# Optimization experiments

Measured on AMD Instinct MI355X. Metric: run time of the kernel, lower is better.

The kernel has to match this reference:

```python
import jax, jax.numpy as jnp
import numpy as np

B, S, H, D = 4, 2048, 12, 64
HIDDEN = H * D  # 768
WINDOW = 64     # config.local_attention // 2
ROPE_THETA = 10000.0  # local_rope_theta for sliding layers


def rotate_half(x):
    d = x.shape[-1] // 2
    return jnp.concatenate([-x[..., d:], x[..., :d]], axis=-1)


def setup_inputs() -> dict:
    key = jax.random.key(0)
    k1, k2, k3 = jax.random.split(key, 3)
    hidden_states = jax.random.normal(k1, (B, S, HIDDEN), dtype=jnp.float32)
    # RoPE tables (HF style): inv_freq over half dims, duplicated
    inv_freq = 1.0 / (ROPE_THETA ** (jnp.arange(0, D, 2, dtype=jnp.float32) / D))  # [D/2]
    pos = jnp.arange(S, dtype=jnp.float32)
    freqs = pos[:, None] * inv_freq[None, :]          # [S, D/2]
    emb = jnp.concatenate([freqs, freqs], axis=-1)    # [S, D]
    cos = jnp.broadcast_to(jnp.cos(emb)[None], (B, S, D))
    sin = jnp.broadcast_to(jnp.sin(emb)[None], (B, S, D))
    # sliding-window additive mask [B,1,S,S]
    idx = jnp.arange(S)
    allowed = jnp.abs(idx[:, None] - idx[None, :]) <= WINDOW
    neg = jnp.finfo(jnp.float32).min
    attention_mask = jnp.broadcast_to(
        jnp.where(allowed, 0.0, neg)[None, None], (B, 1, S, S)
    ).astype(jnp.float32)
    std = 0.02
    Wqkv_w = jax.random.normal(k2, (3 * HIDDEN, HIDDEN), dtype=jnp.float32) * std
    Wo_w = jax.random.normal(k3, (HIDDEN, HIDDEN), dtype=jnp.float32) * std
    return {"hidden_states": hidden_states, "cos": cos, "sin": sin,
            "attention_mask": attention_mask, "Wqkv_w": Wqkv_w, "Wo_w": Wo_w}


def reference(hidden_states, cos, sin, attention_mask, Wqkv_w, Wo_w):
    b, s, _ = hidden_states.shape
    scaling = D ** -0.5
    qkv = hidden_states @ Wqkv_w.T                       # [B,S,3*HIDDEN]
    qkv = qkv.reshape(b, s, 3, H, D)
    q = jnp.transpose(qkv[:, :, 0], (0, 2, 1, 3))        # [B,H,S,D]
    k = jnp.transpose(qkv[:, :, 1], (0, 2, 1, 3))
    v = jnp.transpose(qkv[:, :, 2], (0, 2, 1, 3))
    # RoPE with float32 intermediates (inputs already fp32 here)
    c = cos[:, None].astype(jnp.float32)                 # [B,1,S,D]
    sn = sin[:, None].astype(jnp.float32)
    qf, kf = q.astype(jnp.float32), k.astype(jnp.float32)
    q = (qf * c + rotate_half(qf) * sn).astype(q.dtype)
    k = (kf * c + rotate_half(kf) * sn).astype(k.dtype)
    # SDPA with explicit additive mask
    scores = jnp.einsum('bhqd,bhkd->bhqk', q, k) * scaling + attention_mask
    attn = jax.nn.softmax(scores, axis=-1)
    out = jnp.einsum('bhqk,bhkd->bhqd', attn, v)         # [B,H,S,D]
    out = jnp.transpose(out, (0, 2, 1, 3)).reshape(b, s, HIDDEN)
    return out @ Wo_w.T
```

## Files before the change

kernel.cpp:

```cpp
#include <hip/hip_runtime.h>
#include <math.h>


typedef __attribute__((ext_vector_type(8))) short short8;
typedef __attribute__((ext_vector_type(4))) float floatx4;

constexpr int kB = 4;
constexpr int kS = 2048;
constexpr int kH = 12;
constexpr int kD = 64;
constexpr int kHidden = 768;
constexpr int kQKV = 3 * kHidden;

__device__ __forceinline__ unsigned short f2bf(float f) {
  union { float f; unsigned int u; } x; x.f = f;
  unsigned int r = (x.u + 0x7fffu + ((x.u >> 16) & 1u)) >> 16;
  return (unsigned short)r;
}

__global__ __launch_bounds__(256) void cvt_all(
    const float* __restrict__ h, const float* __restrict__ wqkv,
    const float* __restrict__ wo, unsigned short* __restrict__ hb,
    unsigned short* __restrict__ wqb, unsigned short* __restrict__ wob) {
  constexpr int n1 = kB * kS * kHidden / 4;
  constexpr int n2 = kQKV * kHidden / 4;
  constexpr int n3 = kHidden * kHidden / 4;
  int i = blockIdx.x * 256 + threadIdx.x;
  const float* src;
  unsigned short* dst;
  if (i < n1) {
    src = h; dst = hb;
  } else if (i < n1 + n2) {
    i -= n1; src = wqkv; dst = wqb;
  } else {
    i -= n1 + n2; if (i >= n3) return; src = wo; dst = wob;
  }
  const float4 v = ((const float4*)src)[i];
  ushort4 o;
  o.x = f2bf(v.x); o.y = f2bf(v.y); o.z = f2bf(v.z); o.w = f2bf(v.w);
  ((ushort4*)dst)[i] = o;
}

__device__ __forceinline__ void gload_lds16(const unsigned short* g, unsigned short* l) {
  __builtin_amdgcn_global_load_lds(
      (const __attribute__((address_space(1))) unsigned int*)g,
      (__attribute__((address_space(3))) unsigned int*)l, 16, 0, 0);
}

__global__ __launch_bounds__(512) void gemm_qkv(
    const unsigned short* __restrict__ A,
    const unsigned short* __restrict__ B,
    const float* __restrict__ cosp, const float* __restrict__ sinp,
    unsigned short* __restrict__ Qr, unsigned short* __restrict__ Kr,
    unsigned short* __restrict__ Vt) {
  constexpr int K = kHidden;
  constexpr int NP = 2 * (K / 64);
  __shared__ unsigned short SH[128 * 136];
  unsigned short* Ah0 = SH;
  unsigned short* Ah1 = SH + 4096;
  unsigned short* Bh0 = SH + 8192;
  unsigned short* Bh1 = SH + 12288;

  const int tid = threadIdx.x;
  const int lane = tid & 63;
  const int wave = tid >> 6;
  const int m0 = blockIdx.x * 128;
  const int n0 = blockIdx.y * 128;

  const int sc = wave * 64 + lane;
  const int srow = sc >> 2;
  const int sgc = ((sc & 3) ^ ((srow >> 1) & 3)) * 8;
  const int ldsOff = sc * 8;
  const unsigned short* gA0 = A + (size_t)(m0 + srow) * K + sgc;
  const unsigned short* gB0 = B + (size_t)(n0 + srow) * K + sgc;

  const int wm = wave >> 1, wn = wave & 1;
  const int mr = wm * 32 + (lane & 15);
  const int nr = wn * 64 + (lane & 15);
  const int kq = lane >> 4;

  int aOff[2], bOff[4];
#pragma unroll
  for (int i = 0; i < 2; i++) {
    const int r = mr + i * 16;
    aOff[i] = (r * 4 + (kq ^ ((r >> 1) & 3))) * 8;
  }
#pragma unroll
  for (int j = 0; j < 4; j++) {
    const int r = nr + j * 16;
    bOff[j] = (r * 4 + (kq ^ ((r >> 1) & 3))) * 8;
  }

  floatx4 acc[2][4];
#pragma unroll
  for (int i = 0; i < 2; i++)
#pragma unroll
    for (int j = 0; j < 4; j++) acc[i][j] = (floatx4)(0.f);

  gload_lds16(gA0, &Ah0[ldsOff]);
  gload_lds16(gB0, &Bh0[ldsOff]);

  for (int p = 0; p < NP; ++p) {
    if (p + 1 < NP) {
      const int kn = ((p + 1) >> 1) * 64 + ((p + 1) & 1) * 32;
      unsigned short* Ad = ((p + 1) & 1) ? Ah1 : Ah0;
      unsigned short* Bd = ((p + 1) & 1) ? Bh1 : Bh0;
      gload_lds16(gA0 + kn, &Ad[ldsOff]);
      gload_lds16(gB0 + kn, &Bd[ldsOff]);
      asm volatile("s_waitcnt vmcnt(2)" ::: "memory");
    } else {
      asm volatile("s_waitcnt vmcnt(0)" ::: "memory");
    }
    __builtin_amdgcn_s_barrier();
    __builtin_amdgcn_sched_barrier(0);
    const unsigned short* Asb = (p & 1) ? Ah1 : Ah0;
    const unsigned short* Bsb = (p & 1) ? Bh1 : Bh0;
    short8 af[2], bf[4];
#pragma unroll
    for (int i = 0; i < 2; i++) af[i] = *(const short8*)&Asb[aOff[i]];
#pragma unroll
    for (int j = 0; j < 4; j++) bf[j] = *(const short8*)&Bsb[bOff[j]];
#pragma unroll
    for (int i = 0; i < 2; i++)
#pragma unroll
      for (int j = 0; j < 4; j++)
        acc[i][j] = __builtin_amdgcn_mfma_f32_16x16x32_bf16(af[i], bf[j],
                                                            acc[i][j], 0, 0, 0);
    __builtin_amdgcn_sched_barrier(0);
    __builtin_amdgcn_s_barrier();
  }

  unsigned short (*Obuf)[136] = (unsigned short (*)[136])SH;

  const int region = n0 / kHidden;
  const int b = m0 >> 11, s0 = m0 & 2047;
  const int h0 = (n0 % kHidden) >> 6;
  const int rowL0 = wm * 32 + kq * 4;

  if (region == 2) {
#pragma unroll
    for (int i = 0; i < 2; i++)
#pragma unroll
      for (int r = 0; r < 4; r++) {
        const int rowL = rowL0 + i * 16 + r;
#pragma unroll
        for (int j = 0; j < 4; j++)
          Obuf[wn * 64 + j * 16 + (lane & 15)][rowL] = f2bf(acc[i][j][r]);
      }
    __syncthreads();
#pragma unroll
    for (int it = 0; it < 4; it++) {
      const int t = tid + it * 512;
      const int s8 = t & 15, rowc = t >> 4;
      const int hl = rowc >> 6, d = rowc & 63;
      *(short8*)(Vt + ((size_t)(b * kH + h0 + hl) * kD + d) * kS + s0 + s8 * 8) =
          *(const short8*)&Obuf[rowc][s8 * 8];
    }
  } else {
    unsigned short* dst = (region == 0) ? Qr : Kr;
    const float qscale = (region == 0) ? 0.125f : 1.f;
#pragma unroll
    for (int i = 0; i < 2; i++)
#pragma unroll
      for (int r = 0; r < 4; r++) {
        const int rowL = rowL0 + i * 16 + r;
        const int s = s0 + rowL;
        const float* cs = cosp + ((size_t)(b * kS + s)) * kD;
        const float* sns = sinp + ((size_t)(b * kS + s)) * kD;
#pragma unroll
        for (int jp = 0; jp < 2; jp++) {
          const int colL = wn * 64 + jp * 16 + (lane & 15);
          const int d = colL & 63;
          const float c = cs[d], sn = sns[d];
          const float xlo = acc[i][jp][r], xhi = acc[i][jp + 2][r];
          Obuf[rowL][colL]      = f2bf((xlo * c - xhi * sn) * qscale);
          Obuf[rowL][colL + 32] = f2bf((xhi * c + xlo * sn) * qscale);
        }
      }
    __syncthreads();
#pragma unroll
    for (int it = 0; it < 4; it++) {
      const int t = tid + it * 512;
      const int d8 = t & 7, sl = (t >> 3) & 127, hl = t >> 10;
      *(short8*)(dst + ((size_t)(b * kH + h0 + hl) * kS + s0 + sl) * kD + d8 * 8) =
          *(const short8*)&Obuf[sl][hl * 64 + d8 * 8];
    }
  }
}

__global__ __launch_bounds__(256) void gemm_bf16_nt(
    const unsigned short* __restrict__ A, const unsigned short* __restrict__ B,
    float* __restrict__ C, int M, int N, int K) {
  __shared__ unsigned short As[128 * 64];
  __shared__ unsigned short Bs[64 * 64];

  const int tid = threadIdx.x;
  const int lane = tid & 63;
  const int wave = tid >> 6;
  const int l15 = lane & 15;
  const int m0 = blockIdx.x * 128;
  const int n0 = blockIdx.y * 64;

  int ldsA[4];
  const unsigned short* gA[4];
#pragma unroll
  for (int t = 0; t < 4; t++) {
    const int ci = (wave * 4 + t) * 64 + lane;
    const int row = ci >> 3;
    const int c = (ci & 7) ^ (row & 7);
    ldsA[t] = ci * 8;
    gA[t] = A + (size_t)(m0 + row) * K + c * 8;
  }
  int ldsB[2];
  const unsigned short* gB[2];
#pragma unroll
  for (int t = 0; t < 2; t++) {
    const int ci = (wave * 2 + t) * 64 + lane;
    const int row = ci >> 3;
    const int c = (ci & 7) ^ (row & 7);
    ldsB[t] = ci * 8;
    gB[t] = B + (size_t)(n0 + row) * K + c * 8;
  }

  const int wm = wave >> 1, wn = wave & 1;
  const int mr = wm * 64 + l15;
  const int nr = wn * 32 + l15;
  const int kq = lane >> 4;

  floatx4 acc[4][2];
#pragma unroll
  for (int i = 0; i < 4; i++)
#pragma unroll
    for (int j = 0; j < 2; j++) acc[i][j] = (floatx4)(0.f);

  for (int k0 = 0; k0 < K; k0 += 64) {
    if (k0) __syncthreads();
#pragma unroll
    for (int t = 0; t < 4; t++) gload_lds16(gA[t] + k0, &As[ldsA[t]]);
#pragma unroll
    for (int t = 0; t < 2; t++) gload_lds16(gB[t] + k0, &Bs[ldsB[t]]);
    __syncthreads();
#pragma unroll
    for (int s = 0; s < 2; s++) {
      short8 af[4], bf[2];
#pragma unroll
      for (int i = 0; i < 4; i++)
        af[i] = *(const short8*)&As[(mr + i * 16) * 64 + (((s * 4 + kq) ^ ((mr + i * 16) & 7)) * 8)];
#pragma unroll
      for (int j = 0; j < 2; j++)
        bf[j] = *(const short8*)&Bs[(nr + j * 16) * 64 + (((s * 4 + kq) ^ ((nr + j * 16) & 7)) * 8)];
#pragma unroll
      for (int i = 0; i < 4; i++)
#pragma unroll
        for (int j = 0; j < 2; j++)
          acc[i][j] = __builtin_amdgcn_mfma_f32_16x16x32_bf16(af[i], bf[j],
                                                              acc[i][j], 0, 0, 0);
    }
  }

  const int crow = m0 + wm * 64 + kq * 4;
  const int ccol = n0 + wn * 32 + l15;
#pragma unroll
  for (int i = 0; i < 4; i++)
#pragma unroll
    for (int r = 0; r < 4; r++) {
      float* cp = C + (size_t)(crow + i * 16 + r) * N + ccol;
#pragma unroll
      for (int j = 0; j < 2; j++) cp[j * 16] = acc[i][j][r];
    }
}

constexpr int AQT = 64;

__global__ __launch_bounds__(256) void attn_v4(
    const unsigned short* __restrict__ Qr, const unsigned short* __restrict__ Kr,
    const unsigned short* __restrict__ Vt, unsigned short* __restrict__ out) {
  __shared__ unsigned short Pfrag[4][6][64][8];
  __shared__ float Ssum[2][AQT];

  const int tid = threadIdx.x;
  const int lane = tid & 63;
  const int wave = tid >> 6;
  const int quad = lane >> 4;
  const int l15 = lane & 15;
  const int qbase = blockIdx.x * AQT;
  const int h = blockIdx.y, b = blockIdx.z;
  const int bh = b * kH + h;
  const int kbase = qbase - 64;
  const int tq = wave >> 1;
  const int kh = wave & 1;

  short8 a0[2], a1[2];
#pragma unroll
  for (int qs = 0; qs < 2; qs++) {
    const unsigned short* qsrc =
        Qr + ((size_t)bh * kS + qbase + tq * 32 + qs * 16 + l15) * kD + quad * 8;
    a0[qs] = *(const short8*)qsrc;
    a1[qs] = *(const short8*)(qsrc + 32);
  }

  floatx4 acc[2][6];
  const unsigned short* ksrc = Kr + (size_t)bh * kS * kD;
#pragma unroll
  for (int g = 0; g < 6; g++) {
    int row = kbase + (kh * 6 + g) * 16 + l15;
    row = min(max(row, 0), kS - 1);
    const unsigned short* kp = ksrc + (size_t)row * kD + quad * 8;
    const short8 b0 = *(const short8*)kp;
    const short8 b1 = *(const short8*)(kp + 32);
#pragma unroll
    for (int qs = 0; qs < 2; qs++) {
      floatx4 z = (floatx4)(0.f);
      z = __builtin_amdgcn_mfma_f32_16x16x32_bf16(a0[qs], b0, z, 0, 0, 0);
      z = __builtin_amdgcn_mfma_f32_16x16x32_bf16(a1[qs], b1, z, 0, 0, 0);
      acc[qs][g] = z;
    }
  }

  short8 vf[2][6];
  {
    const unsigned short* vbase = Vt + (size_t)bh * kD * kS;
#pragma unroll
    for (int nt = 0; nt < 2; nt++) {
      const unsigned short* vrow = vbase + (size_t)(kh * 32 + nt * 16 + l15) * kS;
#pragma unroll
      for (int kk = 0; kk < 6; kk++) {
        int s0 = kbase + kk * 32 + quad * 8;
        s0 = min(max(s0, 0), kS - 8);
        vf[nt][kk] = *(const short8*)(vrow + s0);
      }
    }
  }

#pragma unroll
  for (int qs = 0; qs < 2; qs++) {
    const int qgrp = tq * 2 + qs;
#pragma unroll
    for (int r = 0; r < 4; r++) {
      const int q = tq * 32 + qs * 16 + quad * 4 + r;
      float s = 0.f;
#pragma unroll
      for (int g = 0; g < 6; g++) {
        const int key = (kh * 6 + g) * 16 + l15;
        const int kg_ = kbase + key;
        const bool valid = (key >= q) && (key <= q + 128) && (kg_ >= 0) && (kg_ < kS);
        const float e = valid ? __expf(acc[qs][g][r]) : 0.f;
        s += e;
        Pfrag[qgrp][key >> 5][((key >> 3) & 3) * 16 + quad * 4 + r][key & 7] = f2bf(e);
      }
#pragma unroll
      for (int off = 1; off < 16; off <<= 1) s += __shfl_xor(s, off, 64);
      if (l15 == 0) Ssum[kh][q] = s;
    }
  }
  __syncthreads();

  floatx4 o[2][2];
#pragma unroll
  for (int qs = 0; qs < 2; qs++)
#pragma unroll
    for (int nt = 0; nt < 2; nt++) o[qs][nt] = (floatx4)(0.f);
#pragma unroll
  for (int kk = 0; kk < 6; kk++) {
#pragma unroll
    for (int qs = 0; qs < 2; qs++) {
      const short8 pa = *(const short8*)&Pfrag[tq * 2 + qs][kk][lane][0];
      o[qs][0] = __builtin_amdgcn_mfma_f32_16x16x32_bf16(pa, vf[0][kk], o[qs][0], 0, 0, 0);
      o[qs][1] = __builtin_amdgcn_mfma_f32_16x16x32_bf16(pa, vf[1][kk], o[qs][1], 0, 0, 0);
    }
  }

  __syncthreads();
  unsigned short (*Ob)[68] = (unsigned short (*)[68])Pfrag;
#pragma unroll
  for (int qs = 0; qs < 2; qs++)
#pragma unroll
    for (int r = 0; r < 4; r++) {
      const int q = tq * 32 + qs * 16 + quad * 4 + r;
      const float inv = 1.f / (Ssum[0][q] + Ssum[1][q]);
      Ob[q][kh * 32 + l15] = f2bf(o[qs][0][r] * inv);
      Ob[q][kh * 32 + 16 + l15] = f2bf(o[qs][1][r] * inv);
    }
  __syncthreads();
#pragma unroll
  for (int it = 0; it < 2; it++) {
    const int t = tid + it * 256;
    const int q = t >> 3, d8 = t & 7;
    *(short8*)(out + ((size_t)(b * kS + qbase + q)) * kHidden + h * kD + d8 * 8) =
        *(const short8*)&Ob[q][d8 * 8];
  }
}

extern "C" void kernel_launch(void* const* d_in, const int* in_sizes, int n_in,
                              void* d_out, int out_size, void* d_ws,
                              size_t ws_size, hipStream_t stream) {
  const float* hidden = (const float*)d_in[0];
  const float* cosp = (const float*)d_in[1];
  const float* sinp = (const float*)d_in[2];
  const float* wqkv = (const float*)d_in[4];
  const float* wo = (const float*)d_in[5];
  float* out = (float*)d_out;

  const int M = kB * kS;
  const size_t szH = (size_t)M * kHidden;

  unsigned short* hbf = (unsigned short*)d_ws;
  unsigned short* wqkvbf = hbf + szH;
  unsigned short* wobf = wqkvbf + (size_t)kQKV * kHidden;
  unsigned short* attnbf = wobf + (size_t)kHidden * kHidden;
  unsigned short* Qrb = attnbf + szH;
  unsigned short* Krb = Qrb + szH;
  unsigned short* Vtb = Krb + szH;

  const int ncvt = (M * kHidden + kQKV * kHidden + kHidden * kHidden) / 4;
  cvt_all<<<(ncvt + 255) / 256, 256, 0, stream>>>(hidden, wqkv, wo, hbf,
                                                  wqkvbf, wobf);

  dim3 g1(M / 128, kQKV / 128);
  gemm_qkv<<<g1, 512, 0, stream>>>(hbf, wqkvbf, cosp, sinp, Qrb, Krb, Vtb);

  dim3 ga(kS / AQT, kH, kB);
  attn_v4<<<ga, 256, 0, stream>>>(Qrb, Krb, Vtb, attnbf);

  dim3 g2(M / 128, kHidden / 64);
  gemm_bf16_nt<<<g2, 256, 0, stream>>>(attnbf, wobf, out, M, kHidden, kHidden);
}
```

Measured before the change: 206.3 us.

## Load A fragments directly to registers and triple-buffer B in LDS

The QKV GEMM no longer stages the A (hidden states) tile through LDS. Each wave reads its A fragments straight from global memory into registers. The B tile moves to a three-slot LDS ring buffer, which lets the kernel drop the trailing barrier in every k-iteration. The aim is to cut LDS traffic and barrier count, at the cost of uncached, latency-exposed global loads for A that are duplicated across the two waves sharing rows.

```diff
diff --git a/kernel.cpp b/kernel.cpp
--- a/kernel.cpp
+++ b/kernel.cpp
@@ -56,14 +56,11 @@
   constexpr int K = kHidden;
   constexpr int NP = 2 * (K / 64);
   __shared__ unsigned short SH[128 * 136];
-  unsigned short* Ah0 = SH;
-  unsigned short* Ah1 = SH + 4096;
-  unsigned short* Bh0 = SH + 8192;
-  unsigned short* Bh1 = SH + 12288;
 
   const int tid = threadIdx.x;
   const int lane = tid & 63;
   const int wave = tid >> 6;
+  const int l15 = lane & 15;
   const int m0 = blockIdx.x * 128;
   const int n0 = blockIdx.y * 128;
 
@@ -71,65 +68,59 @@
   const int srow = sc >> 2;
   const int sgc = ((sc & 3) ^ ((srow >> 1) & 3)) * 8;
   const int ldsOff = sc * 8;
-  const unsigned short* gA0 = A + (size_t)(m0 + srow) * K + sgc;
   const unsigned short* gB0 = B + (size_t)(n0 + srow) * K + sgc;
 
   const int wm = wave >> 1, wn = wave & 1;
-  const int mr = wm * 32 + (lane & 15);
-  const int nr = wn * 64 + (lane & 15);
+  const int mr = wm * 32 + l15;
+  const int nr = wn * 64 + l15;
   const int kq = lane >> 4;
 
-  int aOff[2], bOff[4];
-#pragma unroll
-  for (int i = 0; i < 2; i++) {
-    const int r = mr + i * 16;
-    aOff[i] = (r * 4 + (kq ^ ((r >> 1) & 3))) * 8;
-  }
+  int bOff[4];
 #pragma unroll
   for (int j = 0; j < 4; j++) {
     const int r = nr + j * 16;
     bOff[j] = (r * 4 + (kq ^ ((r >> 1) & 3))) * 8;
   }
 
+  const unsigned short* aPtr0 = A + (size_t)(m0 + mr) * K + kq * 8;
+  const unsigned short* aPtr1 = A + (size_t)(m0 + mr + 16) * K + kq * 8;
+
   floatx4 acc[2][4];
 #pragma unroll
   for (int i = 0; i < 2; i++)
 #pragma unroll
     for (int j = 0; j < 4; j++) acc[i][j] = (floatx4)(0.f);
 
-  gload_lds16(gA0, &Ah0[ldsOff]);
-  gload_lds16(gB0, &Bh0[ldsOff]);
-
+  gload_lds16(gB0, &SH[ldsOff]);
+
+  int rOff = 0, wOff = 4096;
   for (int p = 0; p < NP; ++p) {
+    const short8 a0 = *(const short8*)aPtr0;
+    const short8 a1 = *(const short8*)aPtr1;
+    aPtr0 += 32; aPtr1 += 32;
     if (p + 1 < NP) {
-      const int kn = ((p + 1) >> 1) * 64 + ((p + 1) & 1) * 32;
-      unsigned short* Ad = ((p + 1) & 1) ? Ah1 : Ah0;
-      unsigned short* Bd = ((p + 1) & 1) ? Bh1 : Bh0;
-      gload_lds16(gA0 + kn, &Ad[ldsOff]);
-      gload_lds16(gB0 + kn, &Bd[ldsOff]);
-      asm volatile("s_waitcnt vmcnt(2)" ::: "memory");
+      gload_lds16(gB0 + (p + 1) * 32, &SH[wOff + ldsOff]);
+      asm volatile("s_waitcnt vmcnt(1)" ::: "memory");
     } else {
       asm volatile("s_waitcnt vmcnt(0)" ::: "memory");
     }
     __builtin_amdgcn_s_barrier();
     __builtin_amdgcn_sched_barrier(0);
-    const unsigned short* Asb = (p & 1) ? Ah1 : Ah0;
-    const unsigned short* Bsb = (p & 1) ? Bh1 : Bh0;
-    short8 af[2], bf[4];
-#pragma unroll
-    for (int i = 0; i < 2; i++) af[i] = *(const short8*)&Asb[aOff[i]];
+    const unsigned short* Bsb = &SH[rOff];
+    short8 bf[4];
 #pragma unroll
     for (int j = 0; j < 4; j++) bf[j] = *(const short8*)&Bsb[bOff[j]];
 #pragma unroll
-    for (int i = 0; i < 2; i++)
-#pragma unroll
-      for (int j = 0; j < 4; j++)
-        acc[i][j] = __builtin_amdgcn_mfma_f32_16x16x32_bf16(af[i], bf[j],
-                                                            acc[i][j], 0, 0, 0);
+    for (int j = 0; j < 4; j++) {
+      acc[0][j] = __builtin_amdgcn_mfma_f32_16x16x32_bf16(a0, bf[j], acc[0][j], 0, 0, 0);
+      acc[1][j] = __builtin_amdgcn_mfma_f32_16x16x32_bf16(a1, bf[j], acc[1][j], 0, 0, 0);
+    }
     __builtin_amdgcn_sched_barrier(0);
-    __builtin_amdgcn_s_barrier();
-  }
-
+    rOff = (rOff == 8192) ? 0 : rOff + 4096;
+    wOff = (wOff == 8192) ? 0 : wOff + 4096;
+  }
+
+  __syncthreads();
   unsigned short (*Obuf)[136] = (unsigned short (*)[136])SH;
 
   const int region = n0 / kHidden;
@@ -145,7 +136,7 @@
         const int rowL = rowL0 + i * 16 + r;
 #pragma unroll
         for (int j = 0; j < 4; j++)
-          Obuf[wn * 64 + j * 16 + (lane & 15)][rowL] = f2bf(acc[i][j][r]);
+          Obuf[wn * 64 + j * 16 + l15][rowL] = f2bf(acc[i][j][r]);
       }
     __syncthreads();
 #pragma unroll
@@ -169,7 +160,7 @@
         const float* sns = sinp + ((size_t)(b * kS + s)) * kD;
 #pragma unroll
         for (int jp = 0; jp < 2; jp++) {
-          const int colL = wn * 64 + jp * 16 + (lane & 15);
+          const int colL = wn * 64 + jp * 16 + l15;
           const int d = colL & 63;
           const float c = cs[d], sn = sns[d];
           const float xlo = acc[i][jp][r], xhi = acc[i][jp + 2][r];
```

New measurement: 234.9 us. 13.9% more time.

## Double-buffer GEMM LDS tiles with half-K stages and async prefetch

Applied to the files above, without the earlier changes.

Restructures the bf16 NT GEMM main loop into 32-wide K stages with two LDS buffers. The next stage's global-to-LDS loads are issued before the current stage's MFMAs, with explicit vmcnt waits and raw barriers, so memory latency overlaps compute. The LDS swizzle changes to suit 32-column rows. The cost is twice as many barriers per K, smaller per-stage MFMA batches, and dependence on hand-placed waitcnt and sched_barrier being correct.

```diff
diff --git a/kernel.cpp b/kernel.cpp
--- a/kernel.cpp
+++ b/kernel.cpp
@@ -191,8 +191,11 @@
 __global__ __launch_bounds__(256) void gemm_bf16_nt(
     const unsigned short* __restrict__ A, const unsigned short* __restrict__ B,
     float* __restrict__ C, int M, int N, int K) {
-  __shared__ unsigned short As[128 * 64];
-  __shared__ unsigned short Bs[64 * 64];
+  __shared__ unsigned short SH[12288];
+  unsigned short* Ah0 = SH;
+  unsigned short* Ah1 = SH + 4096;
+  unsigned short* Bh0 = SH + 8192;
+  unsigned short* Bh1 = SH + 10240;
 
   const int tid = threadIdx.x;
   const int lane = tid & 63;
@@ -200,62 +203,80 @@
   const int l15 = lane & 15;
   const int m0 = blockIdx.x * 128;
   const int n0 = blockIdx.y * 64;
-
-  int ldsA[4];
-  const unsigned short* gA[4];
-#pragma unroll
-  for (int t = 0; t < 4; t++) {
-    const int ci = (wave * 4 + t) * 64 + lane;
-    const int row = ci >> 3;
-    const int c = (ci & 7) ^ (row & 7);
-    ldsA[t] = ci * 8;
-    gA[t] = A + (size_t)(m0 + row) * K + c * 8;
-  }
-  int ldsB[2];
-  const unsigned short* gB[2];
+  const int NP = 2 * (K / 64);
+
+  int ldsA[2];
+  const unsigned short* gA0[2];
 #pragma unroll
   for (int t = 0; t < 2; t++) {
-    const int ci = (wave * 2 + t) * 64 + lane;
-    const int row = ci >> 3;
-    const int c = (ci & 7) ^ (row & 7);
-    ldsB[t] = ci * 8;
-    gB[t] = B + (size_t)(n0 + row) * K + c * 8;
-  }
+    const int sc = wave * 128 + t * 64 + lane;
+    const int srow = sc >> 2;
+    const int sgc = ((sc & 3) ^ ((srow >> 1) & 3)) * 8;
+    ldsA[t] = sc * 8;
+    gA0[t] = A + (size_t)(m0 + srow) * K + sgc;
+  }
+  const int scB = wave * 64 + lane;
+  const int srowB = scB >> 2;
+  const int ldsB = scB * 8;
+  const unsigned short* gB0 =
+      B + (size_t)(n0 + srowB) * K + ((scB & 3) ^ ((srowB >> 1) & 3)) * 8;
 
   const int wm = wave >> 1, wn = wave & 1;
   const int mr = wm * 64 + l15;
   const int nr = wn * 32 + l15;
   const int kq = lane >> 4;
 
+  int aOff[4], bOff[2];
+#pragma unroll
+  for (int i = 0; i < 4; i++) {
+    const int ra = mr + i * 16;
+    aOff[i] = (ra * 4 + (kq ^ ((ra >> 1) & 3))) * 8;
+  }
+#pragma unroll
+  for (int j = 0; j < 2; j++) {
+    const int rb = nr + j * 16;
+    bOff[j] = (rb * 4 + (kq ^ ((rb >> 1) & 3))) * 8;
+  }
+
   floatx4 acc[4][2];
 #pragma unroll
   for (int i = 0; i < 4; i++)
 #pragma unroll
     for (int j = 0; j < 2; j++) acc[i][j] = (floatx4)(0.f);
 
-  for (int k0 = 0; k0 < K; k0 += 64) {
-    if (k0) __syncthreads();
-#pragma unroll
-    for (int t = 0; t < 4; t++) gload_lds16(gA[t] + k0, &As[ldsA[t]]);
-#pragma unroll
-    for (int t = 0; t < 2; t++) gload_lds16(gB[t] + k0, &Bs[ldsB[t]]);
-    __syncthreads();
-#pragma unroll
-    for (int s = 0; s < 2; s++) {
-      short8 af[4], bf[2];
-#pragma unroll
-      for (int i = 0; i < 4; i++)
-        af[i] = *(const short8*)&As[(mr + i * 16) * 64 + (((s * 4 + kq) ^ ((mr + i * 16) & 7)) * 8)];
+  gload_lds16(gA0[0], &Ah0[ldsA[0]]);
+  gload_lds16(gA0[1], &Ah0[ldsA[1]]);
+  gload_lds16(gB0, &Bh0[ldsB]);
+
+  for (int p = 0; p < NP; ++p) {
+    if (p + 1 < NP) {
+      const int kn = (p + 1) * 32;
+      unsigned short* Ad = ((p + 1) & 1) ? Ah1 : Ah0;
+      unsigned short* Bd = ((p + 1) & 1) ? Bh1 : Bh0;
+      gload_lds16(gA0[0] + kn, &Ad[ldsA[0]]);
+      gload_lds16(gA0[1] + kn, &Ad[ldsA[1]]);
+      gload_lds16(gB0 + kn, &Bd[ldsB]);
+      asm volatile("s_waitcnt vmcnt(3)" ::: "memory");
+    } else {
+      asm volatile("s_waitcnt vmcnt(0)" ::: "memory");
+    }
+    __builtin_amdgcn_s_barrier();
+    __builtin_amdgcn_sched_barrier(0);
+    const unsigned short* Asb = (p & 1) ? Ah1 : Ah0;
+    const unsigned short* Bsb = (p & 1) ? Bh1 : Bh0;
+    short8 af[4], bf[2];
+#pragma unroll
+    for (int i = 0; i < 4; i++) af[i] = *(const short8*)&Asb[aOff[i]];
+#pragma unroll
+    for (int j = 0; j < 2; j++) bf[j] = *(const short8*)&Bsb[bOff[j]];
+#pragma unroll
+    for (int i = 0; i < 4; i++)
 #pragma unroll
       for (int j = 0; j < 2; j++)
-        bf[j] = *(const short8*)&Bs[(nr + j * 16) * 64 + (((s * 4 + kq) ^ ((nr + j * 16) & 7)) * 8)];
-#pragma unroll
-      for (int i = 0; i < 4; i++)
-#pragma unroll
-        for (int j = 0; j < 2; j++)
-          acc[i][j] = __builtin_amdgcn_mfma_f32_16x16x32_bf16(af[i], bf[j],
-                                                              acc[i][j], 0, 0, 0);
-    }
+        acc[i][j] = __builtin_amdgcn_mfma_f32_16x16x32_bf16(af[i], bf[j],
+                                                            acc[i][j], 0, 0, 0);
+    __builtin_amdgcn_sched_barrier(0);
+    __builtin_amdgcn_s_barrier();
   }
 
   const int crow = m0 + wm * 64 + kq * 4;
```

New measurement: 209.8 us. Within noise of the previous version (+1.7%).

## Fuse fp32-to-bf16 conversion of hidden states into QKV GEMM A-tile loads

Applied to the files above, without the earlier changes.

The separate conversion pass over the activations is removed. The QKV GEMM now loads fp32 hidden-state tiles into registers, converts them with packed bf16 conversion instructions and writes them to LDS, while the weights still go through direct global-to-LDS loads. This saves a full write and re-read of the bf16 activation copy. In exchange the A operand uses register-staged loads with double the global bytes per tile. The GEMM is launched once per N-tile column, so each fp32 A tile is re-read and re-converted by every such block.

```diff
diff --git a/kernel.cpp b/kernel.cpp
--- a/kernel.cpp
+++ b/kernel.cpp
@@ -18,22 +18,18 @@
   return (unsigned short)r;
 }
 
-__global__ __launch_bounds__(256) void cvt_all(
-    const float* __restrict__ h, const float* __restrict__ wqkv,
-    const float* __restrict__ wo, unsigned short* __restrict__ hb,
+__global__ __launch_bounds__(256) void cvt_wts(
+    const float* __restrict__ wqkv, const float* __restrict__ wo,
     unsigned short* __restrict__ wqb, unsigned short* __restrict__ wob) {
-  constexpr int n1 = kB * kS * kHidden / 4;
   constexpr int n2 = kQKV * kHidden / 4;
   constexpr int n3 = kHidden * kHidden / 4;
   int i = blockIdx.x * 256 + threadIdx.x;
   const float* src;
   unsigned short* dst;
-  if (i < n1) {
-    src = h; dst = hb;
-  } else if (i < n1 + n2) {
-    i -= n1; src = wqkv; dst = wqb;
+  if (i < n2) {
+    src = wqkv; dst = wqb;
   } else {
-    i -= n1 + n2; if (i >= n3) return; src = wo; dst = wob;
+    i -= n2; if (i >= n3) return; src = wo; dst = wob;
   }
   const float4 v = ((const float4*)src)[i];
   ushort4 o;
@@ -48,7 +44,7 @@
 }
 
 __global__ __launch_bounds__(512) void gemm_qkv(
-    const unsigned short* __restrict__ A,
+    const float* __restrict__ A32,
     const unsigned short* __restrict__ B,
     const float* __restrict__ cosp, const float* __restrict__ sinp,
     unsigned short* __restrict__ Qr, unsigned short* __restrict__ Kr,
@@ -71,7 +67,7 @@
   const int srow = sc >> 2;
   const int sgc = ((sc & 3) ^ ((srow >> 1) & 3)) * 8;
   const int ldsOff = sc * 8;
-  const unsigned short* gA0 = A + (size_t)(m0 + srow) * K + sgc;
+  const float* gA32 = A32 + (size_t)(m0 + srow) * K + sgc;
   const unsigned short* gB0 = B + (size_t)(n0 + srow) * K + sgc;
 
   const int wm = wave >> 1, wn = wave & 1;
@@ -97,20 +93,34 @@
 #pragma unroll
     for (int j = 0; j < 4; j++) acc[i][j] = (floatx4)(0.f);
 
-  gload_lds16(gA0, &Ah0[ldsOff]);
+  float4 afc0 = *(const float4*)(gA32);
+  float4 afc1 = *(const float4*)(gA32 + 4);
   gload_lds16(gB0, &Bh0[ldsOff]);
 
   for (int p = 0; p < NP; ++p) {
+    float4 afn0 = make_float4(0.f, 0.f, 0.f, 0.f);
+    float4 afn1 = make_float4(0.f, 0.f, 0.f, 0.f);
     if (p + 1 < NP) {
       const int kn = ((p + 1) >> 1) * 64 + ((p + 1) & 1) * 32;
-      unsigned short* Ad = ((p + 1) & 1) ? Ah1 : Ah0;
+      afn0 = *(const float4*)(gA32 + kn);
+      afn1 = *(const float4*)(gA32 + kn + 4);
       unsigned short* Bd = ((p + 1) & 1) ? Bh1 : Bh0;
-      gload_lds16(gA0 + kn, &Ad[ldsOff]);
       gload_lds16(gB0 + kn, &Bd[ldsOff]);
-      asm volatile("s_waitcnt vmcnt(2)" ::: "memory");
+      asm volatile("s_waitcnt vmcnt(3)" ::: "memory");
     } else {
       asm volatile("s_waitcnt vmcnt(0)" ::: "memory");
     }
+    {
+      unsigned int u0, u1, u2, u3;
+      asm("v_cvt_pk_bf16_f32 %0, %1, %2" : "=v"(u0) : "v"(afc0.x), "v"(afc0.y));
+      asm("v_cvt_pk_bf16_f32 %0, %1, %2" : "=v"(u1) : "v"(afc0.z), "v"(afc0.w));
+      asm("v_cvt_pk_bf16_f32 %0, %1, %2" : "=v"(u2) : "v"(afc1.x), "v"(afc1.y));
+      asm("v_cvt_pk_bf16_f32 %0, %1, %2" : "=v"(u3) : "v"(afc1.z), "v"(afc1.w));
+      unsigned short* Ad = (p & 1) ? Ah1 : Ah0;
+      uint4 pk; pk.x = u0; pk.y = u1; pk.z = u2; pk.w = u3;
+      *(uint4*)&Ad[ldsOff] = pk;
+    }
+    asm volatile("s_waitcnt lgkmcnt(0)" ::: "memory");
     __builtin_amdgcn_s_barrier();
     __builtin_amdgcn_sched_barrier(0);
     const unsigned short* Asb = (p & 1) ? Ah1 : Ah0;
@@ -128,6 +138,7 @@
                                                             acc[i][j], 0, 0, 0);
     __builtin_amdgcn_sched_barrier(0);
     __builtin_amdgcn_s_barrier();
+    afc0 = afn0; afc1 = afn1;
   }
 
   unsigned short (*Obuf)[136] = (unsigned short (*)[136])SH;
@@ -412,12 +423,11 @@
   unsigned short* Krb = Qrb + szH;
   unsigned short* Vtb = Krb + szH;
 
-  const int ncvt = (M * kHidden + kQKV * kHidden + kHidden * kHidden) / 4;
-  cvt_all<<<(ncvt + 255) / 256, 256, 0, stream>>>(hidden, wqkv, wo, hbf,
-                                                  wqkvbf, wobf);
+  const int ncvt = (kQKV * kHidden + kHidden * kHidden) / 4;
+  cvt_wts<<<(ncvt + 255) / 256, 256, 0, stream>>>(wqkv, wo, wqkvbf, wobf);
 
   dim3 g1(M / 128, kQKV / 128);
-  gemm_qkv<<<g1, 512, 0, stream>>>(hbf, wqkvbf, cosp, sinp, Qrb, Krb, Vtb);
+  gemm_qkv<<<g1, 512, 0, stream>>>(hidden, wqkvbf, cosp, sinp, Qrb, Krb, Vtb);
 
   dim3 ga(kS / AQT, kH, kB);
   attn_v4<<<ga, 256, 0, stream>>>(Qrb, Krb, Vtb, attnbf);
```

New measurement: 225.4 us. 1.09x slower.
